# Kernel optimization log

Hardware: AMD Instinct MI355X
Metric: run time of the kernel (lower is better)

The kernel has to match this reference:

```python
import jax, jax.numpy as jnp
import numpy as np
from jax import lax
from jax.scipy.special import logsumexp

B, L, D = 8, 2048, 1330  # esm_dim=1280 + 50
H1, H2, T = 32, 16, 2


def setup_inputs() -> dict:
    key = jax.random.key(0)
    ks = jax.random.split(key, 12)
    x = jax.random.normal(ks[0], (B, L, D), jnp.float32)
    tokens_length = jax.random.randint(ks[1], (B,), 1, L + 1)
    labels = jax.random.randint(ks[2], (B, L), 0, T)
    s = 0.05
    w1 = jax.random.normal(ks[3], (D, H1), jnp.float32) * s
    b1 = jnp.zeros((H1,), jnp.float32)
    conv_w = jax.random.normal(ks[4], (H2, H1, 3), jnp.float32) * s  # OIH
    conv_b = jnp.zeros((H2,), jnp.float32)
    w2 = jax.random.normal(ks[5], (H2, T), jnp.float32) * s
    b2 = jnp.zeros((T,), jnp.float32)
    start_trans = jax.random.normal(ks[6], (T,), jnp.float32) * 0.1
    end_trans = jax.random.normal(ks[7], (T,), jnp.float32) * 0.1
    trans = jax.random.normal(ks[8], (T, T), jnp.float32) * 0.1
    return {"x": x, "tokens_length": tokens_length, "labels": labels,
            "w1": w1, "b1": b1, "conv_w": conv_w, "conv_b": conv_b,
            "w2": w2, "b2": b2, "start_trans": start_trans,
            "end_trans": end_trans, "trans": trans}


def _emission(x, w1, b1, conv_w, conv_b, w2, b2):
    h = x @ w1 + b1                       # [B,L,32] (dropout off: eval)
    h = jnp.transpose(h, (0, 2, 1))       # [B,32,L]
    h = lax.conv_general_dilated(h, conv_w, (1,), [(1, 1)],
                                 dimension_numbers=("NCH", "OIH", "NCH"))
    h = jax.nn.relu(h + conv_b[None, :, None])
    h = jnp.transpose(h, (0, 2, 1))       # [B,L,16]
    return h @ w2 + b2                    # [B,L,2]


def reference(x, tokens_length, labels, w1, b1, conv_w, conv_b, w2, b2,
              start_trans, end_trans, trans):
    em = _emission(x, w1, b1, conv_w, conv_b, w2, b2)    # [B,L,T]
    mask = jnp.arange(L)[None, :] < tokens_length[:, None]  # [B,L] bool

    emT = jnp.transpose(em, (1, 0, 2))   # [L,B,T]
    maskT = mask.T                        # [L,B]
    labT = labels.T                       # [L,B]
    bidx = jnp.arange(B)

    # ---- gold path score (torchcrf _compute_score) ----
    s0 = start_trans[labT[0]] + emT[0][bidx, labT[0]]

    def score_step(carry, inp):
        s, prev = carry
        em_i, lab_i, m_i = inp
        add = trans[prev, lab_i] + jnp.take_along_axis(em_i, lab_i[:, None], axis=1)[:, 0]
        s = s + jnp.where(m_i, add, 0.0)
        prev = jnp.where(m_i, lab_i, prev)
        return (s, prev), None

    (score, _), _ = lax.scan(score_step, (s0, labT[0]),
                             (emT[1:], labT[1:], maskT[1:]))
    seq_ends = tokens_length - 1
    last_tags = labels[bidx, seq_ends]
    score = score + end_trans[last_tags]

    # ---- log-partition (forward algorithm) ----
    a0 = start_trans[None, :] + emT[0]    # [B,T]

    def norm_step(a, inp):
        em_i, m_i = inp
        nxt = logsumexp(a[:, :, None] + trans[None, :, :] + em_i[:, None, :], axis=1)
        return jnp.where(m_i[:, None], nxt, a), None

    a, _ = lax.scan(norm_step, a0, (emT[1:], maskT[1:]))
    norm = logsumexp(a + end_trans[None, :], axis=1)

    llh = score - norm
    neg_loss = -jnp.sum(llh)              # module returns -crf(...), reduction='sum'

    # ---- Viterbi decode ----
    v0 = start_trans[None, :] + emT[0]
    ident = jnp.broadcast_to(jnp.arange(T)[None, :], (B, T))

    def vit_step(v, inp):
        em_i, m_i = inp
        scores = v[:, :, None] + trans[None, :, :]      # [B,prev,cur]
        idx = jnp.argmax(scores, axis=1)                # [B,T]
        best = jnp.max(scores, axis=1) + em_i
        v_new = jnp.where(m_i[:, None], best, v)
        idx = jnp.where(m_i[:, None], idx, ident)       # identity on padded steps
        return v_new, idx

    v, hist = lax.scan(vit_step, v0, (emT[1:], maskT[1:]))  # hist: [L-1,B,T]
    last = jnp.argmax(v + end_trans[None, :], axis=1)       # [B]

    def back_step(tag, h_t):
        prev = jnp.take_along_axis(h_t, tag[:, None], axis=1)[:, 0]
        return prev, prev

    _, tags_front = lax.scan(back_step, last, hist, reverse=True)  # [L-1,B]
    tags = jnp.concatenate([tags_front, last[None, :]], axis=0).T  # [B,L]
    tags = jnp.where(mask, tags, 0)

    return neg_loss, tags


if __name__ == "__main__":
    out = reference(**setup_inputs())
    print(out[0], out[1].shape)
```

## Files before the change

### kernel.cpp

```cpp
#include <hip/hip_runtime.h>

#define LSEQ 2048
#define DIN  1330
#define NB   8
#define SPLITK 7
#define KCH 192
#define K1PAD 1344
#define NSTEP 6

typedef short bf16x8 __attribute__((ext_vector_type(8)));
typedef float f32x4  __attribute__((ext_vector_type(4)));

__device__ __forceinline__ float lsef(float a, float b) {
  float m = fmaxf(a, b);
  float d = fminf(a, b) - m;
  return m + log1pf(__expf(d));
}

__device__ __forceinline__ unsigned short f2bf(float f) {
  unsigned int u = __float_as_uint(f);
  return (unsigned short)((u + 0x7FFFu + ((u >> 16) & 1u)) >> 16);
}

__device__ __forceinline__ float4 lcomp(const float4 A, const float4 B) {
  float4 C;
  C.x = lsef(A.x + B.x, A.y + B.z);
  C.y = lsef(A.x + B.y, A.y + B.w);
  C.z = lsef(A.z + B.x, A.w + B.z);
  C.w = lsef(A.z + B.y, A.w + B.w);
  return C;
}
__device__ __forceinline__ float4 mcomp(const float4 A, const float4 B) {
  float4 C;
  C.x = fmaxf(A.x + B.x, A.y + B.z);
  C.y = fmaxf(A.x + B.y, A.y + B.w);
  C.z = fmaxf(A.z + B.x, A.w + B.z);
  C.w = fmaxf(A.z + B.y, A.w + B.w);
  return C;
}
__device__ __forceinline__ float4 shfl_up4(const float4 v, int d) {
  float4 r;
  r.x = __shfl_up(v.x, d); r.y = __shfl_up(v.y, d);
  r.z = __shfl_up(v.z, d); r.w = __shfl_up(v.w, d);
  return r;
}
__device__ __forceinline__ float4 shfl_dn4(const float4 v, int d) {
  float4 r;
  r.x = __shfl_down(v.x, d); r.y = __shfl_down(v.y, d);
  r.z = __shfl_down(v.z, d); r.w = __shfl_down(v.w, d);
  return r;
}
__device__ __forceinline__ int bmcomp(int A, int B) {
  int c0 = (A >> (B & 1)) & 1;
  int c1 = (A >> ((B >> 1) & 1)) & 1;
  return c0 | (c1 << 1);
}

__global__ __launch_bounds__(256) void k0_wt(
    const float* __restrict__ w1, unsigned short* __restrict__ w1T) {
  const int f = (blockIdx.x * 256 + threadIdx.x) * 4;
  const int h = f / K1PAD, k = f % K1PAD;
  ushort4 v;
  v.x = (k     < DIN) ? f2bf(w1[(long)(k)     * 32 + h]) : (unsigned short)0;
  v.y = (k + 1 < DIN) ? f2bf(w1[(long)(k + 1) * 32 + h]) : (unsigned short)0;
  v.z = (k + 2 < DIN) ? f2bf(w1[(long)(k + 2) * 32 + h]) : (unsigned short)0;
  v.w = (k + 3 < DIN) ? f2bf(w1[(long)(k + 3) * 32 + h]) : (unsigned short)0;
  *(ushort4*)(w1T + f) = v;
}

__global__ __launch_bounds__(256) void k1_mfma(
    const float* __restrict__ x, const unsigned short* __restrict__ w1T,
    float* __restrict__ p) {
  const int tid  = threadIdx.x;
  const int rb   = blockIdx.x / SPLITK;
  const int s    = blockIdx.x % SPLITK;
  const int k0   = s * KCH;

  const int wv   = tid >> 6;
  const int lane = tid & 63;
  const int fr   = lane & 15;
  const int fg   = lane >> 4;

  const long row  = (long)rb * 64 + wv * 16 + fr;
  const float* ap = x + row * DIN;
  const unsigned short* bp0 = w1T + (long)fr * K1PAD;
  const unsigned short* bp1 = w1T + (long)(16 + fr) * K1PAD;

  f32x4 acc0 = {0.f, 0.f, 0.f, 0.f};
  f32x4 acc1 = {0.f, 0.f, 0.f, 0.f};

  #pragma unroll
  for (int t = 0; t < NSTEP; ++t) {
    const int ka = k0 + t * 32 + fg * 8;
    float4 u, v;
    if (ka + 7 < DIN) {
      u = *(const float4*)(ap + ka);
      v = *(const float4*)(ap + ka + 4);
    } else {
      u = make_float4(0.f, 0.f, 0.f, 0.f);
      v = make_float4(0.f, 0.f, 0.f, 0.f);
      if (ka     < DIN) u.x = ap[ka];
      if (ka + 1 < DIN) u.y = ap[ka + 1];
      if (ka + 2 < DIN) u.z = ap[ka + 2];
      if (ka + 3 < DIN) u.w = ap[ka + 3];
      if (ka + 4 < DIN) v.x = ap[ka + 4];
      if (ka + 5 < DIN) v.y = ap[ka + 5];
      if (ka + 6 < DIN) v.z = ap[ka + 6];
      if (ka + 7 < DIN) v.w = ap[ka + 7];
    }
    bf16x8 a;
    a[0] = (short)f2bf(u.x); a[1] = (short)f2bf(u.y);
    a[2] = (short)f2bf(u.z); a[3] = (short)f2bf(u.w);
    a[4] = (short)f2bf(v.x); a[5] = (short)f2bf(v.y);
    a[6] = (short)f2bf(v.z); a[7] = (short)f2bf(v.w);

    const bf16x8 b0 = *(const bf16x8*)(bp0 + ka);
    const bf16x8 b1 = *(const bf16x8*)(bp1 + ka);

    acc0 = __builtin_amdgcn_mfma_f32_16x16x32_bf16(a, b0, acc0, 0, 0, 0);
    acc1 = __builtin_amdgcn_mfma_f32_16x16x32_bf16(a, b1, acc1, 0, 0, 0);
  }

  float* ps = p + (long)s * 524288 + ((long)rb * 64 + wv * 16 + fg * 4) * 32;
  #pragma unroll
  for (int i = 0; i < 4; ++i) {
    ps[(long)i * 32 + fr]      = acc0[i];
    ps[(long)i * 32 + 16 + fr] = acc1[i];
  }
}

__global__ __launch_bounds__(256) void k2_conv(
    const float* __restrict__ p, const float* __restrict__ b1,
    const float* __restrict__ cw, const float* __restrict__ cb,
    const float* __restrict__ w2, const float* __restrict__ b2,
    float* __restrict__ em, int* __restrict__ counter) {
  __shared__ float4 edgeF[4][8];
  __shared__ float4 edgeL[4][8];

  if (blockIdx.x == 0 && threadIdx.x == 0) *counter = 0;

  const int t    = threadIdx.x;
  const int g    = blockIdx.x * 256 + t;
  const int row  = g >> 3;
  const int isub = g & 7;
  const int i0   = isub << 2;
  const int li   = row & (LSEQ - 1);
  const int wv   = t >> 6;
  const int lane = t & 63;

  const float4* p4 = (const float4*)p;
  const float4 bv = ((const float4*)b1)[isub];
  float4 z; z.x = z.y = z.z = z.w = 0.f;

  auto hrow = [&](int r) -> float4 {
    float4 a = p4[(long)r * 8 + isub];
    #pragma unroll
    for (int s = 1; s < SPLITK; ++s) {
      float4 v = p4[(long)s * 131072 + (long)r * 8 + isub];
      a.x += v.x; a.y += v.y; a.z += v.z; a.w += v.w;
    }
    a.x += bv.x; a.y += bv.y; a.z += bv.z; a.w += bv.w;
    return a;
  };

  const float4 hc = hrow(row);

  if (lane < 8)   edgeF[wv][isub] = hc;
  if (lane >= 56) edgeL[wv][isub] = hc;
  __syncthreads();

  float4 hm = shfl_up4(hc, 8);
  float4 hp = shfl_dn4(hc, 8);
  if (lane < 8) {
    if (wv > 0) hm = edgeL[wv - 1][isub];
    else        hm = (li > 0) ? hrow(row - 1) : z;
  }
  if (lane >= 56) {
    if (wv < 3) hp = edgeF[wv + 1][isub];
    else        hp = (li < LSEQ - 1) ? hrow(row + 1) : z;
  }
  if (li == 0)        hm = z;
  if (li == LSEQ - 1) hp = z;

  float s[16];
  #pragma unroll
  for (int o = 0; o < 16; ++o) {
    const float4* wpq = (const float4*)(cw + o * 96 + i0 * 3);
    const float4 wa = wpq[0], wb = wpq[1], wc = wpq[2];
    s[o] = hm.x * wa.x + hc.x * wa.y + hp.x * wa.z
         + hm.y * wa.w + hc.y * wb.x + hp.y * wb.y
         + hm.z * wb.z + hc.z * wb.w + hp.z * wc.x
         + hm.w * wc.y + hc.w * wc.z + hp.w * wc.w;
  }
  #pragma unroll
  for (int o = 0; o < 16; ++o) {
    s[o] += __shfl_xor(s[o], 1, 8);
    s[o] += __shfl_xor(s[o], 2, 8);
    s[o] += __shfl_xor(s[o], 4, 8);
  }
  if (isub == 0) {
    float e0 = b2[0], e1 = b2[1];
    #pragma unroll
    for (int o = 0; o < 16; ++o) {
      float rr = fmaxf(s[o] + cb[o], 0.f);
      e0 += rr * w2[o * 2];
      e1 += rr * w2[o * 2 + 1];
    }
    float2 ev; ev.x = e0; ev.y = e1;
    *(float2*)(em + (long)row * 2) = ev;
  }
}

__global__ __launch_bounds__(256) void k3_crf(
    const float* __restrict__ em, const int* __restrict__ tokens_length,
    const int* __restrict__ labels, const float* __restrict__ start_trans,
    const float* __restrict__ end_trans, const float* __restrict__ trans,
    float* __restrict__ llh, int* __restrict__ counter,
    float* __restrict__ out) {
  __shared__ float sem[LSEQ * 2];
  __shared__ unsigned char hist[LSEQ];
  __shared__ float4 wmat[4];
  __shared__ float wred[4];
  __shared__ int wbm[4];
  __shared__ int s_last;

  const int t = threadIdx.x;
  const int b = blockIdx.x & 7;
  const int role = blockIdx.x >> 3;
  const int len = tokens_length[b];
  const float t00 = trans[0], t01 = trans[1], t10 = trans[2], t11 = trans[3];
  const float st0 = start_trans[0], st1 = start_trans[1];
  const float en0 = end_trans[0], en1 = end_trans[1];
  const int* lab = labels + b * LSEQ;

  const int wv   = t >> 6;
  const int lane = t & 63;

  int lo = t * 8; if (lo < 1) lo = 1;
  int hi = t * 8 + 8; if (hi > len) hi = len;

  const float4 IDENT = make_float4(0.f, -1e30f, -1e30f, 0.f);

  if (role == 0) {
    const float* ge = em + (long)b * LSEQ * 2;

    float sc = 0.f;
    {
      const int base = t * 8;
      #pragma unroll
      for (int k = 0; k < 8; ++k) {
        int l = base + k;
        if (l >= 1 && l < len) {
          int lp = lab[l - 1], lc = lab[l];
          sc += trans[lp * 2 + lc] + ge[2 * l + lc];
        }
      }
    }
    #pragma unroll
    for (int d = 1; d < 64; d <<= 1) sc += __shfl_down(sc, d);

    float4 M = IDENT;
    for (int l = lo; l < hi; ++l) {
      float2 e = *(const float2*)(ge + 2 * l);
      float4 S; S.x = t00 + e.x; S.y = t01 + e.y; S.z = t10 + e.x; S.w = t11 + e.y;
      M = lcomp(M, S);
    }
    #pragma unroll
    for (int d = 1; d < 64; d <<= 1) {
      float4 Mb = shfl_dn4(M, d);
      if (lane + d < 64) M = lcomp(M, Mb);
    }
    if (lane == 0) { wmat[wv] = M; wred[wv] = sc; }
    __syncthreads();

    if (t == 0) {
      float score_part = wred[0] + wred[1] + wred[2] + wred[3];
      float4 Mt = lcomp(lcomp(wmat[0], wmat[1]), lcomp(wmat[2], wmat[3]));
      int lab0 = lab[0];
      float s0 = (lab0 ? st1 : st0) + ge[lab0];
      int labe = lab[len - 1];
      float score = score_part + s0 + (labe ? en1 : en0);
      float a00 = st0 + ge[0], a01 = st1 + ge[1];
      float af0 = lsef(a00 + Mt.x, a01 + Mt.z);
      float af1 = lsef(a00 + Mt.y, a01 + Mt.w);
      float norm = lsef(af0 + en0, af1 + en1);
      llh[b] = score - norm;
      __threadfence();
      int old = atomicAdd(counter, 1);
      if (old == NB - 1) {
        __threadfence();
        const volatile float* lv = llh;
        float ssum = 0.f;
        #pragma unroll
        for (int i = 0; i < NB; ++i) ssum += lv[i];
        out[0] = -ssum;
      }
    }
    return;
  }

  {
    const float4* src4 = (const float4*)(em + (long)b * LSEQ * 2);
    float4* dst4 = (float4*)sem;
    #pragma unroll
    for (int i = t; i < LSEQ * 2 / 4; i += 256) dst4[i] = src4[i];
    #pragma unroll
    for (int l = t; l < LSEQ; l += 256) hist[l] = 2;
  }
  __syncthreads();

  float4 M = IDENT;
  for (int l = lo; l < hi; ++l) {
    float e0 = sem[2 * l], e1 = sem[2 * l + 1];
    float4 S; S.x = t00 + e0; S.y = t01 + e1; S.z = t10 + e0; S.w = t11 + e1;
    M = mcomp(M, S);
  }
  #pragma unroll
  for (int d = 1; d < 64; d <<= 1) {
    float4 Mb = shfl_up4(M, d);
    if (lane >= d) M = mcomp(Mb, M);
  }
  float4 Mprev = shfl_up4(M, 1);
  if (lane == 63) wmat[wv] = M;
  __syncthreads();

  float4 P = IDENT;
  for (int j = 0; j < wv; ++j) P = mcomp(P, wmat[j]);
  float4 E = (lane == 0) ? P : mcomp(P, Mprev);

  {
    const float v00 = st0 + sem[0], v01 = st1 + sem[1];
    float vp0 = fmaxf(v00 + E.x, v01 + E.z);
    float vp1 = fmaxf(v00 + E.y, v01 + E.w);
    for (int l = lo; l < hi; ++l) {
      float e0 = sem[2 * l], e1 = sem[2 * l + 1];
      float s00 = vp0 + t00, s10 = vp1 + t10;
      float s01 = vp0 + t01, s11 = vp1 + t11;
      hist[l] = (unsigned char)((s00 >= s10 ? 0 : 1) | ((s01 >= s11 ? 0 : 1) << 1));
      vp0 = fmaxf(s00, s10) + e0;
      vp1 = fmaxf(s01, s11) + e1;
    }
    if (hi == len && lo < hi)
      s_last = (vp0 + en0 >= vp1 + en1) ? 0 : 1;
    if (t == 0 && len == 1)
      s_last = (v00 + en0 >= v01 + en1) ? 0 : 1;
  }

  int bm = 2;
  {
    int blo = (t == 0) ? 1 : t * 8;
    int bhi = t * 8 + 8;
    int m0 = 0, m1 = 1;
    for (int l = bhi - 1; l >= blo; --l) {
      int h = hist[l];
      m0 = (h >> m0) & 1;
      m1 = (h >> m1) & 1;
    }
    bm = m0 | (m1 << 1);
  }
  #pragma unroll
  for (int d = 1; d < 64; d <<= 1) {
    int bb = __shfl_down(bm, d);
    if (lane + d < 64) bm = bmcomp(bm, bb);
  }
  if (lane == 0) wbm[wv] = bm;
  __syncthreads();

  int suf = 2;
  for (int j = 3; j > wv; --j) suf = bmcomp(wbm[j], suf);
  const int G = bmcomp(bm, suf);
  int gn = __shfl_down(G, 1);
  if (lane == 63) gn = suf;
  const int last = s_last;

  {
    int xv = (t == 255) ? last : ((gn >> last) & 1);
    int blo = (t == 0) ? 1 : t * 8;
    int bhi = t * 8 + 8;
    float* tout = out + 1 + b * LSEQ;
    for (int l = bhi - 1; l >= blo; --l) {
      xv = (hist[l] >> xv) & 1;
      int pidx = l - 1;
      tout[pidx] = (pidx < len) ? (float)xv : 0.0f;
    }
    if (t == 255) tout[LSEQ - 1] = ((LSEQ - 1) < len) ? (float)last : 0.0f;
  }
}

extern "C" void kernel_launch(void* const* d_in, const int* in_sizes, int n_in,
                              void* d_out, int out_size, void* d_ws, size_t ws_size,
                              hipStream_t stream) {
  const float* x  = (const float*)d_in[0];
  const int*   tl = (const int*)d_in[1];
  const int*   lb = (const int*)d_in[2];
  const float* w1 = (const float*)d_in[3];
  const float* b1 = (const float*)d_in[4];
  const float* cw = (const float*)d_in[5];
  const float* cb = (const float*)d_in[6];
  const float* w2 = (const float*)d_in[7];
  const float* b2 = (const float*)d_in[8];
  const float* st = (const float*)d_in[9];
  const float* en = (const float*)d_in[10];
  const float* tr = (const float*)d_in[11];
  float* out = (float*)d_out;
  float* ws  = (float*)d_ws;

  float* p   = ws;
  float* em  = ws + (long)SPLITK * 524288;
  float* llh = em + 32768;
  int*  ctr  = (int*)(llh + 8);
  unsigned short* w1T = (unsigned short*)(llh + 16);

  hipLaunchKernelGGL(k0_wt, dim3(42), dim3(256), 0, stream, w1, w1T);
  hipLaunchKernelGGL(k1_mfma, dim3(256 * SPLITK), dim3(256), 0, stream, x, w1T, p);
  hipLaunchKernelGGL(k2_conv, dim3(512), dim3(256), 0, stream, p, b1, cw, cb, w2, b2, em, ctr);
  hipLaunchKernelGGL(k3_crf, dim3(16), dim3(256), 0, stream, em, tl, lb, st, en, tr, llh, ctr, out);
}
```

Baseline: 58.02 us.

## Stage x tiles through LDS with async global_load_lds double buffering

The first GEMM kernel now copies its slice of w1T into shared memory once per block, and streams x tiles into double-buffered LDS using the direct global-to-LDS load builtin, prefetching the next tile while computing the current one. The aim is coalesced 16-byte loads of x across rows, replacing the strided per-lane row reads, and overlap of loads with MFMA work. It adds a __syncthreads per k-step and a scalar fallback path for the tail that crosses DIN.

```diff
diff --git a/kernel.cpp b/kernel.cpp
--- a/kernel.cpp
+++ b/kernel.cpp
@@ -6,10 +6,11 @@
 #define SPLITK 7
 #define KCH 192
 #define K1PAD 1344
-#define NSTEP 6
+#define NTILE 6
 
 typedef short bf16x8 __attribute__((ext_vector_type(8)));
 typedef float f32x4  __attribute__((ext_vector_type(4)));
+typedef unsigned short ushort8v __attribute__((ext_vector_type(8)));
 
 __device__ __forceinline__ float lsef(float a, float b) {
   float m = fmaxf(a, b);
@@ -55,6 +56,10 @@
   int c1 = (A >> ((B >> 1) & 1)) & 1;
   return c0 | (c1 << 1);
 }
+
+#define GLDS(g, l) __builtin_amdgcn_global_load_lds( \
+    (const __attribute__((address_space(1))) void*)(g), \
+    (__attribute__((address_space(3))) void*)(l), 16, 0, 0)
 
 __global__ __launch_bounds__(256) void k0_wt(
     const float* __restrict__ w1, unsigned short* __restrict__ w1T) {
@@ -71,57 +76,85 @@
 __global__ __launch_bounds__(256) void k1_mfma(
     const float* __restrict__ x, const unsigned short* __restrict__ w1T,
     float* __restrict__ p) {
-  const int tid  = threadIdx.x;
-  const int rb   = blockIdx.x / SPLITK;
-  const int s    = blockIdx.x % SPLITK;
-  const int k0   = s * KCH;
+  __shared__ float xb[2][8 * 256];
+  __shared__ unsigned short wb[32 * 200];
+
+  const int tid = threadIdx.x;
+  const int rb  = blockIdx.x / SPLITK;
+  const int s   = blockIdx.x % SPLITK;
+  const int k0  = s * KCH;
+  const long row0 = (long)rb * 64;
 
   const int wv   = tid >> 6;
   const int lane = tid & 63;
   const int fr   = lane & 15;
   const int fg   = lane >> 4;
 
-  const long row  = (long)rb * 64 + wv * 16 + fr;
-  const float* ap = x + row * DIN;
-  const unsigned short* bp0 = w1T + (long)fr * K1PAD;
-  const unsigned short* bp1 = w1T + (long)(16 + fr) * K1PAD;
+  #pragma unroll
+  for (int i = 0; i < 3; ++i) {
+    const int idx = (i * 256 + tid) * 8;
+    const int h  = idx / KCH;
+    const int kk = idx % KCH;
+    const ushort8v v = *(const ushort8v*)(w1T + (long)h * K1PAD + k0 + kk);
+    *(ushort8v*)(wb + h * 200 + kk) = v;
+  }
+
+  auto stage_x = [&](int tt, int bb) {
+    const bool tail = (s == SPLITK - 1) && (tt == NTILE - 1);
+    #pragma unroll
+    for (int c = 0; c < 2; ++c) {
+      const int sl = wv * 2 + c;
+      const int gk = k0 + tt * 32 + sl * 4;
+      float* ldst = &xb[bb][sl * 256];
+      if (!tail || sl < 4) {
+        const float* gsrc = x + (row0 + lane) * DIN + gk;
+        GLDS(gsrc, ldst);
+      } else {
+        const float* rp = x + (row0 + lane) * DIN;
+        float4 vv;
+        vv.x = (gk     < DIN) ? rp[gk]     : 0.f;
+        vv.y = (gk + 1 < DIN) ? rp[gk + 1] : 0.f;
+        vv.z = (gk + 2 < DIN) ? rp[gk + 2] : 0.f;
+        vv.w = (gk + 3 < DIN) ? rp[gk + 3] : 0.f;
+        *(float4*)(ldst + lane * 4) = vv;
+      }
+    }
+  };
+
+  const unsigned short* bp0 = wb + fr * 200;
+  const unsigned short* bp1 = wb + (16 + fr) * 200;
 
   f32x4 acc0 = {0.f, 0.f, 0.f, 0.f};
   f32x4 acc1 = {0.f, 0.f, 0.f, 0.f};
 
-  #pragma unroll
-  for (int t = 0; t < NSTEP; ++t) {
-    const int ka = k0 + t * 32 + fg * 8;
-    float4 u, v;
-    if (ka + 7 < DIN) {
-      u = *(const float4*)(ap + ka);
-      v = *(const float4*)(ap + ka + 4);
-    } else {
-      u = make_float4(0.f, 0.f, 0.f, 0.f);
-      v = make_float4(0.f, 0.f, 0.f, 0.f);
-      if (ka     < DIN) u.x = ap[ka];
-      if (ka + 1 < DIN) u.y = ap[ka + 1];
-      if (ka + 2 < DIN) u.z = ap[ka + 2];
-      if (ka + 3 < DIN) u.w = ap[ka + 3];
-      if (ka + 4 < DIN) v.x = ap[ka + 4];
-      if (ka + 5 < DIN) v.y = ap[ka + 5];
-      if (ka + 6 < DIN) v.z = ap[ka + 6];
-      if (ka + 7 < DIN) v.w = ap[ka + 7];
-    }
+  stage_x(0, 0);
+  __syncthreads();
+
+  #pragma unroll 1
+  for (int t = 0; t < NTILE; ++t) {
+    const int bi = t & 1;
+    if (t + 1 < NTILE) stage_x(t + 1, bi ^ 1);
+
+    const int rofs = (wv * 16 + fr) * 4;
+    const float4 u = *(const float4*)(&xb[bi][(2 * fg)     * 256 + rofs]);
+    const float4 v = *(const float4*)(&xb[bi][(2 * fg + 1) * 256 + rofs]);
     bf16x8 a;
     a[0] = (short)f2bf(u.x); a[1] = (short)f2bf(u.y);
     a[2] = (short)f2bf(u.z); a[3] = (short)f2bf(u.w);
     a[4] = (short)f2bf(v.x); a[5] = (short)f2bf(v.y);
     a[6] = (short)f2bf(v.z); a[7] = (short)f2bf(v.w);
 
-    const bf16x8 b0 = *(const bf16x8*)(bp0 + ka);
-    const bf16x8 b1 = *(const bf16x8*)(bp1 + ka);
+    const int wofs = t * 32 + fg * 8;
+    const bf16x8 b0 = *(const bf16x8*)(bp0 + wofs);
+    const bf16x8 b1 = *(const bf16x8*)(bp1 + wofs);
 
     acc0 = __builtin_amdgcn_mfma_f32_16x16x32_bf16(a, b0, acc0, 0, 0, 0);
     acc1 = __builtin_amdgcn_mfma_f32_16x16x32_bf16(a, b1, acc1, 0, 0, 0);
-  }
-
-  float* ps = p + (long)s * 524288 + ((long)rb * 64 + wv * 16 + fg * 4) * 32;
+
+    __syncthreads();
+  }
+
+  float* ps = p + (long)s * 524288 + (row0 + wv * 16 + fg * 4) * 32;
   #pragma unroll
   for (int i = 0; i < 4; ++i) {
     ps[(long)i * 32 + fr]      = acc0[i];
```

Measured after the change: 59.76 us. 3.0% more time.
